# Optimization experiments

Measured on AMD Instinct MI355X. Metric: run time of the kernel, lower is better.

Reference implementation:

```python
import jax, jax.numpy as jnp
import numpy as np

EPSILON = 0.01  # from init_kwargs

def setup_inputs() -> dict:
    key = jax.random.key(0)
    k1, k2, k3, k4 = jax.random.split(key, 4)
    N, E, D = 100000, 3200000, 4
    x = jax.random.normal(k1, (N, D), dtype=jnp.float32)
    edge_index = jax.random.randint(k2, (2, E), 0, N, dtype=jnp.int32)
    boo_values = jax.random.normal(k3, (E, D, D), dtype=jnp.float32)
    mask = jnp.ones((N, 1), dtype=jnp.float32)
    diag = jax.random.uniform(k4, (N, D), dtype=jnp.float32)
    return {"x": x, "edge_index": edge_index, "boo_values": boo_values,
            "mask": mask, "diag": diag}

def reference(x, edge_index, boo_values, mask, diag):
    # y = eps*diag*x + A @ (diag * (A^T @ x)), A blocked-sparse with
    # per-edge blocks A_{row,col} = boo_values[e] in R^{DxD}.
    N = x.shape[0]
    row, col = edge_index[0], edge_index[1]
    # spmv_t (A^T x): gather x at row i, message A_ij^T x_i, scatter-add to col j
    msg_t = jnp.einsum('eji,ej->ei', boo_values, x[row])  # [E, D]
    AT_x = jax.ops.segment_sum(msg_t, col, num_segments=N) * mask  # [N, D]
    eps_x = EPSILON * x
    AT_x = AT_x * diag
    eps_x = eps_x * diag
    # spmv (A v): gather v at col j, message A_ij v_j, scatter-add to row i
    msg = jnp.einsum('eij,ej->ei', boo_values, AT_x[col])  # [E, D]
    A_AT_x = jax.ops.segment_sum(msg, row, num_segments=N) * mask  # [N, D]
    return eps_x + A_AT_x
```

## Files before the change

kernel.cpp:

```cpp
#include <hip/hip_runtime.h>

#define EPSILON 0.01f

#define BLK    256
#define SLICE  2048
#define SLOG   11
#define PCH    26
#define BCH    2048
#define MAXS   64


__global__ void init_cursors(int* cur1, int* cur2, int S, int cap) {
    int t = threadIdx.x;
    if (t < S) { cur1[t] = t * cap; cur2[t] = t * cap; }
}

__global__ void __launch_bounds__(BLK) bin_kernel(
    const int* __restrict__ row, const int* __restrict__ col,
    int2* __restrict__ bins1, int2* __restrict__ bins2,
    int* __restrict__ cur1, int* __restrict__ cur2,
    long long E, int S)
{
    __shared__ int h1[MAXS], h2[MAXS], b1[MAXS], b2[MAXS];
    const int t = threadIdx.x;
    if (t < S) { h1[t] = 0; h2[t] = 0; }
    __syncthreads();

    long long start = (long long)blockIdx.x * BCH;
    long long end   = start + BCH; if (end > E) end = E;

    for (long long t0 = start + (long long)t * 4; t0 < end; t0 += (long long)BLK * 4) {
        if (t0 + 4 <= end) {
            int4 c = *reinterpret_cast<const int4*>(col + t0);
            int4 r = *reinterpret_cast<const int4*>(row + t0);
            atomicAdd(&h1[c.x >> SLOG], 1); atomicAdd(&h1[c.y >> SLOG], 1);
            atomicAdd(&h1[c.z >> SLOG], 1); atomicAdd(&h1[c.w >> SLOG], 1);
            atomicAdd(&h2[r.x >> SLOG], 1); atomicAdd(&h2[r.y >> SLOG], 1);
            atomicAdd(&h2[r.z >> SLOG], 1); atomicAdd(&h2[r.w >> SLOG], 1);
        } else {
            for (long long e = t0; e < end; ++e) {
                atomicAdd(&h1[col[e] >> SLOG], 1);
                atomicAdd(&h2[row[e] >> SLOG], 1);
            }
        }
    }
    __syncthreads();
    if (t < S) {
        b1[t] = atomicAdd(&cur1[t], h1[t]); h1[t] = 0;
        b2[t] = atomicAdd(&cur2[t], h2[t]); h2[t] = 0;
    }
    __syncthreads();

    for (long long t0 = start + (long long)t * 4; t0 < end; t0 += (long long)BLK * 4) {
        long long lim4 = (t0 + 4 <= end) ? t0 + 4 : end;
        if (t0 + 4 <= end) {
            int4 c = *reinterpret_cast<const int4*>(col + t0);
            int4 r = *reinterpret_cast<const int4*>(row + t0);
            int cc[4] = {c.x, c.y, c.z, c.w};
            int rr[4] = {r.x, r.y, r.z, r.w};
            #pragma unroll
            for (int u = 0; u < 4; ++u) {
                int s1 = cc[u] >> SLOG;
                int i1 = b1[s1] + atomicAdd(&h1[s1], 1);
                bins1[i1] = make_int2((int)(t0 + u), ((cc[u] & (SLICE - 1)) << 17) | rr[u]);
                int s2 = rr[u] >> SLOG;
                int i2 = b2[s2] + atomicAdd(&h2[s2], 1);
                bins2[i2] = make_int2((int)(t0 + u), ((rr[u] & (SLICE - 1)) << 17) | cc[u]);
            }
        } else {
            for (long long e = t0; e < lim4; ++e) {
                int cv = col[e], rv = row[e];
                int s1 = cv >> SLOG;
                int i1 = b1[s1] + atomicAdd(&h1[s1], 1);
                bins1[i1] = make_int2((int)e, ((cv & (SLICE - 1)) << 17) | rv);
                int s2 = rv >> SLOG;
                int i2 = b2[s2] + atomicAdd(&h2[s2], 1);
                bins2[i2] = make_int2((int)e, ((rv & (SLICE - 1)) << 17) | cv);
            }
        }
    }
}

template<int PASS, int STAGED>
__global__ void __launch_bounds__(BLK) pass_kernel(
    const float4* __restrict__ boo,
    const int2*   __restrict__ bins,
    const int*    __restrict__ cur,
    const float4* __restrict__ src,
    const float*  __restrict__ mask,
    float*        __restrict__ dst,
    int N, int cap, int P)
{
    __shared__ float acc[SLICE * 4];

    const int s    = blockIdx.x / P;
    const int p    = blockIdx.x - s * P;
    const int base = s << SLOG;
    const int lim  = min(SLICE, N - base);

    for (int i = threadIdx.x; i < SLICE * 4; i += BLK) acc[i] = 0.0f;
    __syncthreads();

    const int cnt = cur[s] - s * cap;
    const int lo  = (int)((long long)cnt * p / P);
    const int hi  = (int)((long long)cnt * (p + 1) / P);
    const int2* __restrict__ bin = bins + (size_t)s * cap;

    for (int i = lo + (int)threadIdx.x; i < hi; i += BLK) {
        int2 rec = bin[i];
        const float4* B = boo + (long long)rec.x * 4;
        float4 b0 = B[0], b1 = B[1], b2 = B[2], b3 = B[3];
        float4 v = src[rec.y & 0x1FFFF];
        float* a = acc + (((unsigned)rec.y) >> 17) * 4;
        if (PASS == 1) {
            atomicAdd(a + 0, b0.x*v.x + b1.x*v.y + b2.x*v.z + b3.x*v.w);
            atomicAdd(a + 1, b0.y*v.x + b1.y*v.y + b2.y*v.z + b3.y*v.w);
            atomicAdd(a + 2, b0.z*v.x + b1.z*v.y + b2.z*v.z + b3.z*v.w);
            atomicAdd(a + 3, b0.w*v.x + b1.w*v.y + b2.w*v.z + b3.w*v.w);
        } else {
            atomicAdd(a + 0, b0.x*v.x + b0.y*v.y + b0.z*v.z + b0.w*v.w);
            atomicAdd(a + 1, b1.x*v.x + b1.y*v.y + b1.z*v.z + b1.w*v.w);
            atomicAdd(a + 2, b2.x*v.x + b2.y*v.y + b2.z*v.z + b2.w*v.w);
            atomicAdd(a + 3, b3.x*v.x + b3.y*v.y + b3.z*v.z + b3.w*v.w);
        }
    }
    __syncthreads();

    if (STAGED) {
        float* st = dst + (size_t)blockIdx.x * (SLICE * 4);
        for (int f = threadIdx.x; f < lim * 4; f += BLK) st[f] = acc[f];
    } else if (PASS == 1) {
        for (int f = threadIdx.x; f < lim * 4; f += BLK)
            unsafeAtomicAdd(dst + ((long long)base * 4 + f), acc[f]);
    } else {
        for (int f = threadIdx.x; f < lim * 4; f += BLK) {
            float mv = mask[base + (f >> 2)];
            unsafeAtomicAdd(dst + ((long long)base * 4 + f), acc[f] * mv);
        }
    }
}

__global__ void __launch_bounds__(BLK) mid_staged_kernel(
    const float4* __restrict__ stage,
    const float4* __restrict__ d4,
    const float*  __restrict__ mask,
    float4* __restrict__ v4,
    int N, int P)
{
    int n = blockIdx.x * BLK + threadIdx.x;
    if (n >= N) return;
    int s = n >> SLOG, local = n & (SLICE - 1);
    const float4* t = stage + ((size_t)s * P) * SLICE + local;
    float4 a = make_float4(0.f, 0.f, 0.f, 0.f);
    for (int p = 0; p < P; ++p) {
        float4 u = t[(size_t)p * SLICE];
        a.x += u.x; a.y += u.y; a.z += u.z; a.w += u.w;
    }
    float4 dv = d4[n];
    float  m  = mask[n];
    a.x *= dv.x * m; a.y *= dv.y * m; a.z *= dv.z * m; a.w *= dv.w * m;
    v4[n] = a;
}

__global__ void __launch_bounds__(BLK) fin_staged_kernel(
    const float4* __restrict__ stage,
    const float4* __restrict__ x4,
    const float4* __restrict__ d4,
    const float*  __restrict__ mask,
    float4* __restrict__ out4,
    int N, int P)
{
    int n = blockIdx.x * BLK + threadIdx.x;
    if (n >= N) return;
    int s = n >> SLOG, local = n & (SLICE - 1);
    const float4* t = stage + ((size_t)s * P) * SLICE + local;
    float4 a = make_float4(0.f, 0.f, 0.f, 0.f);
    for (int p = 0; p < P; ++p) {
        float4 u = t[(size_t)p * SLICE];
        a.x += u.x; a.y += u.y; a.z += u.z; a.w += u.w;
    }
    float4 xv = x4[n];
    float4 dv = d4[n];
    float  m  = mask[n];
    float4 o;
    o.x = EPSILON * xv.x * dv.x + a.x * m;
    o.y = EPSILON * xv.y * dv.y + a.y * m;
    o.z = EPSILON * xv.z * dv.z + a.z * m;
    o.w = EPSILON * xv.w * dv.w + a.w * m;
    out4[n] = o;
}

__global__ void __launch_bounds__(BLK) mid_atomic_kernel(
    const float4* __restrict__ x4,
    const float4* __restrict__ d4,
    const float*  __restrict__ mask,
    float4* __restrict__ atx,
    float4* __restrict__ out4,
    int N)
{
    int n = blockIdx.x * BLK + threadIdx.x;
    if (n >= N) return;
    float4 a  = atx[n];
    float4 dv = d4[n];
    float  m  = mask[n];
    a.x *= dv.x * m; a.y *= dv.y * m; a.z *= dv.z * m; a.w *= dv.w * m;
    atx[n] = a;
    float4 xv = x4[n];
    float4 o;
    o.x = EPSILON * xv.x * dv.x; o.y = EPSILON * xv.y * dv.y;
    o.z = EPSILON * xv.z * dv.z; o.w = EPSILON * xv.w * dv.w;
    out4[n] = o;
}

__global__ void __launch_bounds__(256) spmvt_kernel(
    const float4* __restrict__ boo, const int* __restrict__ row,
    const int* __restrict__ col, const float* __restrict__ x,
    float* __restrict__ ATx, long long E)
{
    long long t = (long long)blockIdx.x * blockDim.x + threadIdx.x;
    long long e = t >> 2;
    int j = (int)(t & 3);
    if (e >= E) return;
    float4 b = boo[e * 4 + j];
    int r = row[e];
    float xj = x[r * 4 + j];
    float4 p;
    p.x = b.x * xj; p.y = b.y * xj; p.z = b.z * xj; p.w = b.w * xj;
    p.x += __shfl_xor(p.x, 1); p.y += __shfl_xor(p.y, 1);
    p.z += __shfl_xor(p.z, 1); p.w += __shfl_xor(p.w, 1);
    p.x += __shfl_xor(p.x, 2); p.y += __shfl_xor(p.y, 2);
    p.z += __shfl_xor(p.z, 2); p.w += __shfl_xor(p.w, 2);
    float v = (j == 0) ? p.x : (j == 1) ? p.y : (j == 2) ? p.z : p.w;
    int c = col[e];
    unsafeAtomicAdd(&ATx[c * 4 + j], v);
}

__global__ void __launch_bounds__(256) spmv_kernel(
    const float4* __restrict__ boo, const int* __restrict__ row,
    const int* __restrict__ col, const float* __restrict__ vv,
    const float* __restrict__ mask, float* __restrict__ out, long long E)
{
    long long t = (long long)blockIdx.x * blockDim.x + threadIdx.x;
    long long e = t >> 2;
    int i = (int)(t & 3);
    if (e >= E) return;
    float4 b = boo[e * 4 + i];
    int c = col[e];
    const float4* v4 = (const float4*)vv;
    float4 v = v4[c];
    float mi = b.x * v.x + b.y * v.y + b.z * v.z + b.w * v.w;
    int r = row[e];
    float mr = mask[r];
    unsafeAtomicAdd(&out[r * 4 + i], mi * mr);
}

extern "C" void kernel_launch(void* const* d_in, const int* in_sizes, int n_in,
                              void* d_out, int out_size, void* d_ws, size_t ws_size,
                              hipStream_t stream) {
    const float* x    = (const float*)d_in[0];
    const int*   ei   = (const int*)d_in[1];
    const float* boo  = (const float*)d_in[2];
    const float* mask = (const float*)d_in[3];
    const float* diag = (const float*)d_in[4];
    float* out = (float*)d_out;

    int N = in_sizes[0] / 4;
    long long E = in_sizes[1] / 2;
    const int* row = ei;
    const int* col = ei + E;

    int S = (N + SLICE - 1) >> SLOG;
    int cap = (int)((E + S - 1) / S);
    cap += cap * 3 / 10;
    cap = (cap + 255) & ~255;

    size_t o_v   = 0;
    size_t o_cur = ((size_t)N * 16 + 255) & ~(size_t)255;
    size_t o_b1  = o_cur + 1024;
    size_t szb   = (size_t)S * cap * 8;
    size_t o_b2  = o_b1 + szb;
    size_t o_st  = o_b2 + szb;
    size_t szst  = (size_t)S * PCH * SLICE * 16;

    bool ok   = (S <= MAXS) && (N <= (1 << 17)) && ((E & 3) == 0 || true);
    int  tier = (!ok) ? 3 : (ws_size >= o_st + szst) ? 1
                          : (ws_size >= o_st)        ? 2 : 3;

    float* v     = (float*)((char*)d_ws + o_v);
    int*   cur1  = (int*)((char*)d_ws + o_cur);
    int*   cur2  = cur1 + 128;
    int2*  bins1 = (int2*)((char*)d_ws + o_b1);
    int2*  bins2 = (int2*)((char*)d_ws + o_b2);
    float* stage = (float*)((char*)d_ws + o_st);

    const int gNode = (N + BLK - 1) / BLK;
    const int gBin  = (int)((E + BCH - 1) / BCH);
    const int gPass = S * PCH;

    if (tier <= 2) {
        init_cursors<<<1, MAXS, 0, stream>>>(cur1, cur2, S, cap);
        bin_kernel<<<gBin, BLK, 0, stream>>>(row, col, bins1, bins2, cur1, cur2, E, S);
        if (tier == 1) {
            pass_kernel<1, 1><<<gPass, BLK, 0, stream>>>(
                (const float4*)boo, bins1, cur1, (const float4*)x, mask, stage, N, cap, PCH);
            mid_staged_kernel<<<gNode, BLK, 0, stream>>>(
                (const float4*)stage, (const float4*)diag, mask, (float4*)v, N, PCH);
            pass_kernel<2, 1><<<gPass, BLK, 0, stream>>>(
                (const float4*)boo, bins2, cur2, (const float4*)v, mask, stage, N, cap, PCH);
            fin_staged_kernel<<<gNode, BLK, 0, stream>>>(
                (const float4*)stage, (const float4*)x, (const float4*)diag, mask,
                (float4*)out, N, PCH);
        } else {
            hipMemsetAsync(v, 0, (size_t)N * 16, stream);
            pass_kernel<1, 0><<<gPass, BLK, 0, stream>>>(
                (const float4*)boo, bins1, cur1, (const float4*)x, mask, v, N, cap, PCH);
            mid_atomic_kernel<<<gNode, BLK, 0, stream>>>(
                (const float4*)x, (const float4*)diag, mask, (float4*)v, (float4*)out, N);
            pass_kernel<2, 0><<<gPass, BLK, 0, stream>>>(
                (const float4*)boo, bins2, cur2, (const float4*)v, mask, out, N, cap, PCH);
        }
    } else {
        hipMemsetAsync(v, 0, (size_t)N * 16, stream);
        long long T = E * 4;
        int gEdge = (int)((T + BLK - 1) / BLK);
        spmvt_kernel<<<gEdge, BLK, 0, stream>>>(
            (const float4*)boo, row, col, x, v, E);
        mid_atomic_kernel<<<gNode, BLK, 0, stream>>>(
            (const float4*)x, (const float4*)diag, mask, (float4*)v, (float4*)out, N);
        spmv_kernel<<<gEdge, BLK, 0, stream>>>(
            (const float4*)boo, row, col, v, mask, out, E);
    }
}
```

Measured before the change: 544.4 us.

## Use per-wavefront histograms in binning and unroll pass loop by two edges

The binning kernel now gives each wavefront its own shared-memory histogram and its own write offsets, which cuts LDS atomic contention. Each block also handles twice as many edges, halving the number of global cursor atomics. The pass kernel processes two bin records per iteration so more boo block loads are in flight at once. The cost is more shared memory and more registers per thread, plus fewer binning blocks in flight.

```diff
diff --git a/kernel.cpp b/kernel.cpp
--- a/kernel.cpp
+++ b/kernel.cpp
@@ -3,11 +3,13 @@
 #define EPSILON 0.01f
 
 #define BLK    256
+#define NW     4
 #define SLICE  2048
 #define SLOG   11
 #define PCH    26
-#define BCH    2048
+#define BCH    4096
 #define MAXS   64
+#define HP     65
 
 
 __global__ void init_cursors(int* cur1, int* cur2, int S, int cap) {
@@ -21,9 +23,12 @@
     int* __restrict__ cur1, int* __restrict__ cur2,
     long long E, int S)
 {
-    __shared__ int h1[MAXS], h2[MAXS], b1[MAXS], b2[MAXS];
+    __shared__ int h1[NW * HP], h2[NW * HP];
+    __shared__ int bw1[NW * HP], bw2[NW * HP];
     const int t = threadIdx.x;
-    if (t < S) { h1[t] = 0; h2[t] = 0; }
+    const int w = t >> 6;
+
+    for (int i = t; i < NW * HP; i += BLK) { h1[i] = 0; h2[i] = 0; }
     __syncthreads();
 
     long long start = (long long)blockIdx.x * BCH;
@@ -33,26 +38,44 @@
         if (t0 + 4 <= end) {
             int4 c = *reinterpret_cast<const int4*>(col + t0);
             int4 r = *reinterpret_cast<const int4*>(row + t0);
-            atomicAdd(&h1[c.x >> SLOG], 1); atomicAdd(&h1[c.y >> SLOG], 1);
-            atomicAdd(&h1[c.z >> SLOG], 1); atomicAdd(&h1[c.w >> SLOG], 1);
-            atomicAdd(&h2[r.x >> SLOG], 1); atomicAdd(&h2[r.y >> SLOG], 1);
-            atomicAdd(&h2[r.z >> SLOG], 1); atomicAdd(&h2[r.w >> SLOG], 1);
+            atomicAdd(&h1[w * HP + (c.x >> SLOG)], 1);
+            atomicAdd(&h1[w * HP + (c.y >> SLOG)], 1);
+            atomicAdd(&h1[w * HP + (c.z >> SLOG)], 1);
+            atomicAdd(&h1[w * HP + (c.w >> SLOG)], 1);
+            atomicAdd(&h2[w * HP + (r.x >> SLOG)], 1);
+            atomicAdd(&h2[w * HP + (r.y >> SLOG)], 1);
+            atomicAdd(&h2[w * HP + (r.z >> SLOG)], 1);
+            atomicAdd(&h2[w * HP + (r.w >> SLOG)], 1);
         } else {
             for (long long e = t0; e < end; ++e) {
-                atomicAdd(&h1[col[e] >> SLOG], 1);
-                atomicAdd(&h2[row[e] >> SLOG], 1);
+                atomicAdd(&h1[w * HP + (col[e] >> SLOG)], 1);
+                atomicAdd(&h2[w * HP + (row[e] >> SLOG)], 1);
             }
         }
     }
     __syncthreads();
+
     if (t < S) {
-        b1[t] = atomicAdd(&cur1[t], h1[t]); h1[t] = 0;
-        b2[t] = atomicAdd(&cur2[t], h2[t]); h2[t] = 0;
-    }
+        int a0 = h1[0 * HP + t], a1 = h1[1 * HP + t],
+            a2 = h1[2 * HP + t], a3 = h1[3 * HP + t];
+        int g = atomicAdd(&cur1[t], a0 + a1 + a2 + a3);
+        bw1[0 * HP + t] = g;
+        bw1[1 * HP + t] = g + a0;
+        bw1[2 * HP + t] = g + a0 + a1;
+        bw1[3 * HP + t] = g + a0 + a1 + a2;
+        int c0 = h2[0 * HP + t], c1 = h2[1 * HP + t],
+            c2 = h2[2 * HP + t], c3 = h2[3 * HP + t];
+        int g2 = atomicAdd(&cur2[t], c0 + c1 + c2 + c3);
+        bw2[0 * HP + t] = g2;
+        bw2[1 * HP + t] = g2 + c0;
+        bw2[2 * HP + t] = g2 + c0 + c1;
+        bw2[3 * HP + t] = g2 + c0 + c1 + c2;
+    }
+    __syncthreads();
+    for (int i = t; i < NW * HP; i += BLK) { h1[i] = 0; h2[i] = 0; }
     __syncthreads();
 
     for (long long t0 = start + (long long)t * 4; t0 < end; t0 += (long long)BLK * 4) {
-        long long lim4 = (t0 + 4 <= end) ? t0 + 4 : end;
         if (t0 + 4 <= end) {
             int4 c = *reinterpret_cast<const int4*>(col + t0);
             int4 r = *reinterpret_cast<const int4*>(row + t0);
@@ -61,20 +84,20 @@
             #pragma unroll
             for (int u = 0; u < 4; ++u) {
                 int s1 = cc[u] >> SLOG;
-                int i1 = b1[s1] + atomicAdd(&h1[s1], 1);
+                int i1 = bw1[w * HP + s1] + atomicAdd(&h1[w * HP + s1], 1);
                 bins1[i1] = make_int2((int)(t0 + u), ((cc[u] & (SLICE - 1)) << 17) | rr[u]);
                 int s2 = rr[u] >> SLOG;
-                int i2 = b2[s2] + atomicAdd(&h2[s2], 1);
+                int i2 = bw2[w * HP + s2] + atomicAdd(&h2[w * HP + s2], 1);
                 bins2[i2] = make_int2((int)(t0 + u), ((rr[u] & (SLICE - 1)) << 17) | cc[u]);
             }
         } else {
-            for (long long e = t0; e < lim4; ++e) {
+            for (long long e = t0; e < end; ++e) {
                 int cv = col[e], rv = row[e];
                 int s1 = cv >> SLOG;
-                int i1 = b1[s1] + atomicAdd(&h1[s1], 1);
+                int i1 = bw1[w * HP + s1] + atomicAdd(&h1[w * HP + s1], 1);
                 bins1[i1] = make_int2((int)e, ((cv & (SLICE - 1)) << 17) | rv);
                 int s2 = rv >> SLOG;
-                int i2 = b2[s2] + atomicAdd(&h2[s2], 1);
+                int i2 = bw2[w * HP + s2] + atomicAdd(&h2[w * HP + s2], 1);
                 bins2[i2] = make_int2((int)e, ((rv & (SLICE - 1)) << 17) | cv);
             }
         }
@@ -106,10 +129,7 @@
     const int hi  = (int)((long long)cnt * (p + 1) / P);
     const int2* __restrict__ bin = bins + (size_t)s * cap;
 
-    for (int i = lo + (int)threadIdx.x; i < hi; i += BLK) {
-        int2 rec = bin[i];
-        const float4* B = boo + (long long)rec.x * 4;
-        float4 b0 = B[0], b1 = B[1], b2 = B[2], b3 = B[3];
+    auto accum = [&](int2 rec, float4 b0, float4 b1, float4 b2, float4 b3) {
         float4 v = src[rec.y & 0x1FFFF];
         float* a = acc + (((unsigned)rec.y) >> 17) * 4;
         if (PASS == 1) {
@@ -123,6 +143,23 @@
             atomicAdd(a + 2, b2.x*v.x + b2.y*v.y + b2.z*v.z + b2.w*v.w);
             atomicAdd(a + 3, b3.x*v.x + b3.y*v.y + b3.z*v.z + b3.w*v.w);
         }
+    };
+
+    int i = lo + (int)threadIdx.x;
+    for (; i + BLK < hi; i += 2 * BLK) {
+        int2 ra = bin[i];
+        int2 rb = bin[i + BLK];
+        const float4* Ba = boo + (long long)ra.x * 4;
+        const float4* Bb = boo + (long long)rb.x * 4;
+        float4 a0 = Ba[0], a1 = Ba[1], a2 = Ba[2], a3 = Ba[3];
+        float4 c0 = Bb[0], c1 = Bb[1], c2 = Bb[2], c3 = Bb[3];
+        accum(ra, a0, a1, a2, a3);
+        accum(rb, c0, c1, c2, c3);
+    }
+    if (i < hi) {
+        int2 ra = bin[i];
+        const float4* Ba = boo + (long long)ra.x * 4;
+        accum(ra, Ba[0], Ba[1], Ba[2], Ba[3]);
     }
     __syncthreads();
 
@@ -282,7 +319,7 @@
     size_t o_st  = o_b2 + szb;
     size_t szst  = (size_t)S * PCH * SLICE * 16;
 
-    bool ok   = (S <= MAXS) && (N <= (1 << 17)) && ((E & 3) == 0 || true);
+    bool ok   = (S <= MAXS) && (N <= (1 << 17));
     int  tier = (!ok) ? 3 : (ws_size >= o_st + szst) ? 1
                           : (ws_size >= o_st)        ? 2 : 3;
 
```

Result: faster. 524.5 us (-3.6%).
